# Optimization experiments

Hardware: AMD Instinct MI355X
Metric: run time of the kernel (lower is better)

Reference implementation:

```python
import jax, jax.numpy as jnp
import numpy as np

N = 50000
NEG_SLOPE = 0.2


def add_self_loops(edge_index, n):
    loop = jnp.arange(n, dtype=edge_index.dtype)
    return jnp.concatenate([edge_index, jnp.stack([loop, loop])], axis=1)


def gatv2_conv(x, edge_index, Wl, bl, Wr, br, att, bias):
    """PyG GATv2Conv (share_weights=False, concat=True, add_self_loops applied by caller).
    x: [N, Fin]; edge_index: [2, E] with row0=src(j), row1=dst(i); att: [H, D].
    Returns (out [N, H*D], alpha [E, H])."""
    src, dst = edge_index[0], edge_index[1]
    H, D = att.shape
    n = x.shape[0]
    xl = (x @ Wl + bl).reshape(n, H, D)   # source-side transform
    xr = (x @ Wr + br).reshape(n, H, D)   # target-side transform
    e = jax.nn.leaky_relu(xl[src] + xr[dst], NEG_SLOPE)        # [E, H, D]
    logit = jnp.einsum('ehd,hd->eh', e, att)                    # [E, H]
    # segment softmax over edges grouped by target node
    lmax = jax.ops.segment_max(logit, dst, num_segments=n)      # [N, H]
    ex = jnp.exp(logit - lmax[dst])
    denom = jax.ops.segment_sum(ex, dst, num_segments=n)
    alpha = ex / denom[dst]                                     # [E, H]
    out = jax.ops.segment_sum(alpha[:, :, None] * xl[src], dst, num_segments=n)  # [N, H, D]
    return out.reshape(n, H * D) + bias, alpha


def setup_inputs() -> dict:
    key = jax.random.key(0)
    ks = jax.random.split(key, 16)
    E = 400000
    x = jax.random.normal(ks[0], (N, 23), dtype=jnp.float32)
    edge_index = jax.random.randint(ks[1], (2, E), 0, N, dtype=jnp.int64)
    H1, D1 = 8, 64
    F1 = H1 * D1  # 512
    s = 0.1
    return {
        'x': x,
        'edge_index': edge_index,
        'Wl1': jax.random.normal(ks[2], (23, F1), dtype=jnp.float32) * s,
        'bl1': jnp.zeros((F1,), jnp.float32),
        'Wr1': jax.random.normal(ks[3], (23, F1), dtype=jnp.float32) * s,
        'br1': jnp.zeros((F1,), jnp.float32),
        'att1': jax.random.normal(ks[4], (H1, D1), dtype=jnp.float32) * s,
        'bias1': jnp.zeros((F1,), jnp.float32),
        'Wl2': jax.random.normal(ks[5], (F1, 1), dtype=jnp.float32) * s,
        'bl2': jnp.zeros((1,), jnp.float32),
        'Wr2': jax.random.normal(ks[6], (F1, 1), dtype=jnp.float32) * s,
        'br2': jnp.zeros((1,), jnp.float32),
        'att2': jax.random.normal(ks[7], (1, 1), dtype=jnp.float32) * s,
        'bias2': jnp.zeros((1,), jnp.float32),
    }


def reference(x, edge_index, Wl1, bl1, Wr1, br1, att1, bias1,
              Wl2, bl2, Wr2, br2, att2, bias2):
    ei = add_self_loops(edge_index, N)
    h, _ = gatv2_conv(x, ei, Wl1, bl1, Wr1, br1, att1, bias1)
    h = jax.nn.relu(h)
    h, alpha = gatv2_conv(h, ei, Wl2, bl2, Wr2, br2, att2, bias2)
    return h, alpha
```

## Files before the change

kernel.cpp:

```cpp
#include <hip/hip_runtime.h>
#include <math.h>

#define NN 50000
#define E0 400000
#define EE 450000
#define FF 512
#define G1 2048
#define NPB 25
#define EPB 220
#define WAVES_TOTAL (G1 * 4)
#define MAXD 64
#define LOG2E 1.44269504f

typedef _Float16 h2 __attribute__((ext_vector_type(2)));

__device__ __forceinline__ h2 uas_h2(unsigned u) { union { unsigned u; h2 h; } c; c.u = u; return c.h; }
__device__ __forceinline__ unsigned h2as_u(h2 h) { union { unsigned u; h2 h; } c; c.h = h; return c.u; }
__device__ __forceinline__ unsigned packh(float a, float b) {
    h2 hh = { (_Float16)a, (_Float16)b };
    return h2as_u(hh);
}
__device__ __forceinline__ float leaky(float v) { return fmaxf(v, 0.2f * v); }

__global__ __launch_bounds__(256) void k_predeg(
    const float* __restrict__ x,
    const float* __restrict__ Wl1, const float* __restrict__ bl1,
    const float* __restrict__ Wr1, const float* __restrict__ br1,
    const int* __restrict__ ei,
    unsigned* __restrict__ xlh, unsigned* __restrict__ xrh,
    int* __restrict__ cnt, int* __restrict__ src_sl)
{
    __shared__ unsigned sxh[NPB * 12];
    int b = blockIdx.x, t = threadIdx.x;

    {
        int e0 = b * EPB;
        int e1 = e0 + EPB; if (e1 > EE) e1 = EE;
        for (int e = e0 + t; e < e1; e += 256) {
            int src, dst;
            if (e < E0) { src = ei[e]; dst = ei[E0 + e]; }
            else        { src = e - E0; dst = src; }
            int p = atomicAdd(&cnt[dst], 1);
            if (p < MAXD) src_sl[(size_t)dst * MAXD + p] = src;
        }
    }

    int i0 = b * NPB;
    int i1 = i0 + NPB; if (i1 > NN) i1 = NN;
    int nnod = i1 - i0;
    for (int k = t; k < nnod * 12; k += 256) {
        int n = k / 12, j = k - n * 12;
        const float* row = x + (size_t)(i0 + n) * 23;
        float f0 = row[2 * j];
        float f1 = (2 * j + 1 < 23) ? row[2 * j + 1] : 0.f;
        sxh[n * 12 + j] = packh(f0, f1);
    }

    int c0 = 2 * t, c1 = 2 * t + 1;
    h2 wl0[12], wl1[12], wr0[12], wr1[12];
#pragma unroll
    for (int j = 0; j < 12; j++) {
        int r0 = 2 * j, r1 = 2 * j + 1;
        float a, b2;
        a = Wl1[r0 * FF + c0]; b2 = (r1 < 23) ? Wl1[r1 * FF + c0] : 0.f;
        wl0[j] = (h2){ (_Float16)a, (_Float16)b2 };
        a = Wl1[r0 * FF + c1]; b2 = (r1 < 23) ? Wl1[r1 * FF + c1] : 0.f;
        wl1[j] = (h2){ (_Float16)a, (_Float16)b2 };
        a = Wr1[r0 * FF + c0]; b2 = (r1 < 23) ? Wr1[r1 * FF + c0] : 0.f;
        wr0[j] = (h2){ (_Float16)a, (_Float16)b2 };
        a = Wr1[r0 * FF + c1]; b2 = (r1 < 23) ? Wr1[r1 * FF + c1] : 0.f;
        wr1[j] = (h2){ (_Float16)a, (_Float16)b2 };
    }
    float bl0 = bl1[c0], bl1s = bl1[c1];
    float br0 = br1[c0], br1s = br1[c1];
    __syncthreads();

    const uint4* S = (const uint4*)sxh;
    for (int n = 0; n < nnod; n++) {
        uint4 xa = S[n * 3 + 0];
        uint4 xb = S[n * 3 + 1];
        uint4 xc = S[n * 3 + 2];
        h2 xv[12] = { uas_h2(xa.x), uas_h2(xa.y), uas_h2(xa.z), uas_h2(xa.w),
                      uas_h2(xb.x), uas_h2(xb.y), uas_h2(xb.z), uas_h2(xb.w),
                      uas_h2(xc.x), uas_h2(xc.y), uas_h2(xc.z), uas_h2(xc.w) };
        float al0 = bl0, al1 = bl1s, ar0 = br0, ar1 = br1s;
#pragma unroll
        for (int j = 0; j < 12; j++) {
            al0 = __builtin_amdgcn_fdot2(wl0[j], xv[j], al0, false);
            al1 = __builtin_amdgcn_fdot2(wl1[j], xv[j], al1, false);
            ar0 = __builtin_amdgcn_fdot2(wr0[j], xv[j], ar0, false);
            ar1 = __builtin_amdgcn_fdot2(wr1[j], xv[j], ar1, false);
        }
        xlh[(size_t)(i0 + n) * 256 + t] = packh(al0, al1);
        xrh[(size_t)(i0 + n) * 256 + t] = packh(ar0, ar1);
    }
}

__global__ __launch_bounds__(256) void k_layer1(
    const uint4* __restrict__ xlh, const uint4* __restrict__ xrh,
    const float* __restrict__ att, const float* __restrict__ bias1,
    const float* __restrict__ Wl2, const float* __restrict__ bl2,
    const float* __restrict__ Wr2, const float* __restrict__ br2,
    const int* __restrict__ cnt, const int* __restrict__ src_sl,
    float* __restrict__ xl2, float* __restrict__ xr2)
{
    int t = threadIdx.x;
    int l = t & 63;
    int wid = blockIdx.x * 4 + (t >> 6);

    float4 atA = ((const float4*)att)[2 * l];
    float4 atB = ((const float4*)att)[2 * l + 1];
    h2 a6_0 = { (_Float16)(0.6f * LOG2E * atA.x), (_Float16)(0.6f * LOG2E * atA.y) };
    h2 a6_1 = { (_Float16)(0.6f * LOG2E * atA.z), (_Float16)(0.6f * LOG2E * atA.w) };
    h2 a6_2 = { (_Float16)(0.6f * LOG2E * atB.x), (_Float16)(0.6f * LOG2E * atB.y) };
    h2 a6_3 = { (_Float16)(0.6f * LOG2E * atB.z), (_Float16)(0.6f * LOG2E * atB.w) };
    h2 a4_0 = { (_Float16)(0.4f * LOG2E * atA.x), (_Float16)(0.4f * LOG2E * atA.y) };
    h2 a4_1 = { (_Float16)(0.4f * LOG2E * atA.z), (_Float16)(0.4f * LOG2E * atA.w) };
    h2 a4_2 = { (_Float16)(0.4f * LOG2E * atB.x), (_Float16)(0.4f * LOG2E * atB.y) };
    h2 a4_3 = { (_Float16)(0.4f * LOG2E * atB.z), (_Float16)(0.4f * LOG2E * atB.w) };
    float bl2v = bl2[0], br2v = br2[0];

    for (int i = wid; i < NN; i += WAVES_TOTAL) {
        uint4 xq = xrh[(size_t)i * 64 + l];
        h2 q0 = uas_h2(xq.x), q1 = uas_h2(xq.y), q2 = uas_h2(xq.z), q3 = uas_h2(xq.w);

        float s = 0.f;
        h2 A0 = { 0, 0 }, A1 = { 0, 0 }, A2 = { 0, 0 }, A3 = { 0, 0 };

        int dg = cnt[i]; if (dg > MAXD) dg = MAXD;
        int myj = (l < dg) ? src_sl[(size_t)i * MAXD + l] : 0;

        int j0 = __builtin_amdgcn_readlane(myj, 0);
        uint4 r0 = xlh[(size_t)j0 * 64 + l];
        uint4 r1 = r0;
        if (dg > 1) r1 = xlh[(size_t)__builtin_amdgcn_readlane(myj, 1) * 64 + l];

        for (int p = 0; p < dg; p++) {
            uint4 rn = r0;
            if (p + 2 < dg)
                rn = xlh[(size_t)__builtin_amdgcn_readlane(myj, p + 2) * 64 + l];

            h2 p0 = uas_h2(r0.x), p1 = uas_h2(r0.y), p2 = uas_h2(r0.z), p3 = uas_h2(r0.w);
            h2 t0 = p0 + q0, t1 = p1 + q1, t2 = p2 + q2, t3 = p3 + q3;
            h2 b0 = uas_h2(h2as_u(t0) & 0x7fff7fffu);
            h2 b1 = uas_h2(h2as_u(t1) & 0x7fff7fffu);
            h2 b2 = uas_h2(h2as_u(t2) & 0x7fff7fffu);
            h2 b3 = uas_h2(h2as_u(t3) & 0x7fff7fffu);
            float part = 0.f;
            part = __builtin_amdgcn_fdot2(a6_0, t0, part, false);
            part = __builtin_amdgcn_fdot2(a4_0, b0, part, false);
            part = __builtin_amdgcn_fdot2(a6_1, t1, part, false);
            part = __builtin_amdgcn_fdot2(a4_1, b1, part, false);
            part = __builtin_amdgcn_fdot2(a6_2, t2, part, false);
            part = __builtin_amdgcn_fdot2(a4_2, b2, part, false);
            part = __builtin_amdgcn_fdot2(a6_3, t3, part, false);
            part = __builtin_amdgcn_fdot2(a4_3, b3, part, false);
            part += __shfl_xor(part, 1, 64);
            part += __shfl_xor(part, 2, 64);
            part += __shfl_xor(part, 4, 64);
            float wv = exp2f(part);
            s += wv;
            _Float16 wh = (_Float16)wv;
            h2 w2 = { wh, wh };
            A0 += w2 * p0;
            A1 += w2 * p1;
            A2 += w2 * p2;
            A3 += w2 * p3;
            r0 = r1; r1 = rn;
        }

        float inv = 1.f / s;
        float4 bA = ((const float4*)bias1)[2 * l];
        float4 bB = ((const float4*)bias1)[2 * l + 1];
        float h0 = fmaxf(fmaf((float)A0[0], inv, bA.x), 0.f);
        float h1 = fmaxf(fmaf((float)A0[1], inv, bA.y), 0.f);
        float h2v = fmaxf(fmaf((float)A1[0], inv, bA.z), 0.f);
        float h3 = fmaxf(fmaf((float)A1[1], inv, bA.w), 0.f);
        float h4 = fmaxf(fmaf((float)A2[0], inv, bB.x), 0.f);
        float h5 = fmaxf(fmaf((float)A2[1], inv, bB.y), 0.f);
        float h6 = fmaxf(fmaf((float)A3[0], inv, bB.z), 0.f);
        float h7 = fmaxf(fmaf((float)A3[1], inv, bB.w), 0.f);

        float4 wlA = ((const float4*)Wl2)[2 * l];
        float4 wlB = ((const float4*)Wl2)[2 * l + 1];
        float4 wrA = ((const float4*)Wr2)[2 * l];
        float4 wrB = ((const float4*)Wr2)[2 * l + 1];
        float pl = h0 * wlA.x + h1 * wlA.y + h2v * wlA.z + h3 * wlA.w
                 + h4 * wlB.x + h5 * wlB.y + h6 * wlB.z + h7 * wlB.w;
        float pr = h0 * wrA.x + h1 * wrA.y + h2v * wrA.z + h3 * wrA.w
                 + h4 * wrB.x + h5 * wrB.y + h6 * wrB.z + h7 * wrB.w;
#pragma unroll
        for (int o = 32; o > 0; o >>= 1) {
            pl += __shfl_xor(pl, o, 64);
            pr += __shfl_xor(pr, o, 64);
        }
        if (l == 0) {
            xl2[i] = pl + bl2v;
            xr2[i] = pr + br2v;
        }
    }
}

__global__ void k_layer2a(const float* __restrict__ xl2, const float* __restrict__ xr2,
                          const float* __restrict__ att2, const float* __restrict__ bias2,
                          const int* __restrict__ cnt, const int* __restrict__ src_sl,
                          float* __restrict__ out, float* __restrict__ invs)
{
    int i = blockIdx.x * blockDim.x + threadIdx.x;
    if (i >= NN) return;
    int dg = cnt[i]; if (dg > MAXD) dg = MAXD;
    const int* sp = src_sl + (size_t)i * MAXD;
    float xri = xr2[i];
    float a2l = att2[0] * LOG2E;
    float s = 0.f, num = 0.f;
    for (int p = 0; p < dg; p++) {
        float v = xl2[sp[p]];
        float w = exp2f(leaky(v + xri) * a2l);
        s += w;
        num = fmaf(w, v, num);
    }
    out[i] = num / s + bias2[0];
    invs[i] = 1.f / s;
}

__global__ void k_layer2b(const float* __restrict__ xl2, const float* __restrict__ xr2,
                          const float* __restrict__ att2, const int* __restrict__ ei,
                          const float* __restrict__ invs, float* __restrict__ out)
{
    int e = blockIdx.x * blockDim.x + threadIdx.x;
    if (e >= EE) return;
    int src, dst;
    if (e < E0) { src = ei[e]; dst = ei[E0 + e]; }
    else        { src = e - E0; dst = src; }
    float a2l = att2[0] * LOG2E;
    float lg = leaky(xl2[src] + xr2[dst]) * a2l;
    out[NN + e] = exp2f(lg) * invs[dst];
}

extern "C" void kernel_launch(void* const* d_in, const int* in_sizes, int n_in,
                              void* d_out, int out_size, void* d_ws, size_t ws_size,
                              hipStream_t stream)
{
    const float* x     = (const float*)d_in[0];
    const int*   ei    = (const int*)d_in[1];
    const float* Wl1   = (const float*)d_in[2];
    const float* bl1   = (const float*)d_in[3];
    const float* Wr1   = (const float*)d_in[4];
    const float* br1   = (const float*)d_in[5];
    const float* att1  = (const float*)d_in[6];
    const float* bias1 = (const float*)d_in[7];
    const float* Wl2   = (const float*)d_in[8];
    const float* bl2   = (const float*)d_in[9];
    const float* Wr2   = (const float*)d_in[10];
    const float* br2   = (const float*)d_in[11];
    const float* att2  = (const float*)d_in[12];
    const float* bias2 = (const float*)d_in[13];
    float* out = (float*)d_out;

    char* ws = (char*)d_ws;
    unsigned* xlh  = (unsigned*)ws; ws += (size_t)NN * 256 * 4;
    unsigned* xrh  = (unsigned*)ws; ws += (size_t)NN * 256 * 4;
    float* xl2     = (float*)ws;    ws += (size_t)NN * 4;
    float* xr2     = (float*)ws;    ws += (size_t)NN * 4;
    float* invs    = (float*)ws;    ws += (size_t)NN * 4;
    int* cnt       = (int*)ws;      ws += (size_t)NN * 4;
    int* src_sl    = (int*)ws;      ws += (size_t)NN * MAXD * 4;

    hipMemsetAsync(cnt, 0, (size_t)NN * 4, stream);

    k_predeg<<<G1, 256, 0, stream>>>(x, Wl1, bl1, Wr1, br1, ei, xlh, xrh,
                                     cnt, src_sl);
    k_layer1<<<G1, 256, 0, stream>>>((const uint4*)xlh, (const uint4*)xrh,
                                     att1, bias1, Wl2, bl2, Wr2, br2,
                                     cnt, src_sl, xl2, xr2);
    k_layer2a<<<(NN + 255) / 256, 256, 0, stream>>>(xl2, xr2, att2, bias2,
                                                    cnt, src_sl, out, invs);
    k_layer2b<<<(EE + 255) / 256, 256, 0, stream>>>(xl2, xr2, att2, ei, invs, out);
}
```

Baseline: 228.0 us.

## Quantize source-side features to int8 with per-node scale for gather

The source-side transform xl is now stored as int8 with one per-node float scale instead of fp16. This halves the bytes gathered per edge in the layer-1 aggregation. Values are dequantized in registers with a magic-number fp16 trick and then multiplied by the scale. This adds a shared-memory pass and per-node max reduction in the producer kernel, and trades accuracy for bandwidth.

```diff
diff --git a/kernel.cpp b/kernel.cpp
--- a/kernel.cpp
+++ b/kernel.cpp
@@ -27,11 +27,15 @@
     const float* __restrict__ Wl1, const float* __restrict__ bl1,
     const float* __restrict__ Wr1, const float* __restrict__ br1,
     const int* __restrict__ ei,
-    unsigned* __restrict__ xlh, unsigned* __restrict__ xrh,
+    unsigned short* __restrict__ xlq, float* __restrict__ xlsc,
+    unsigned* __restrict__ xrh,
     int* __restrict__ cnt, int* __restrict__ src_sl)
 {
     __shared__ unsigned sxh[NPB * 12];
+    __shared__ unsigned sal[NPB * 256];
+    __shared__ float swmax[NPB * 4];
     int b = blockIdx.x, t = threadIdx.x;
+    int l = t & 63, w = t >> 6;
 
     {
         int e0 = b * EPB;
@@ -91,13 +95,32 @@
             ar0 = __builtin_amdgcn_fdot2(wr0[j], xv[j], ar0, false);
             ar1 = __builtin_amdgcn_fdot2(wr1[j], xv[j], ar1, false);
         }
-        xlh[(size_t)(i0 + n) * 256 + t] = packh(al0, al1);
         xrh[(size_t)(i0 + n) * 256 + t] = packh(ar0, ar1);
+        sal[n * 256 + t] = packh(al0, al1);
+        float m = fmaxf(fabsf(al0), fabsf(al1));
+#pragma unroll
+        for (int o = 32; o > 0; o >>= 1) m = fmaxf(m, __shfl_xor(m, o, 64));
+        if (l == 0) swmax[n * 4 + w] = m;
+    }
+    __syncthreads();
+
+    for (int n = 0; n < nnod; n++) {
+        float rm = fmaxf(fmaxf(swmax[n * 4 + 0], swmax[n * 4 + 1]),
+                         fmaxf(swmax[n * 4 + 2], swmax[n * 4 + 3]));
+        rm = fmaxf(rm, 1e-8f);
+        float qi = 127.f / rm;
+        h2 alp = uas_h2(sal[n * 256 + t]);
+        int q0 = (int)rintf(fminf(fmaxf((float)alp[0] * qi, -127.f), 127.f));
+        int q1 = (int)rintf(fminf(fmaxf((float)alp[1] * qi, -127.f), 127.f));
+        xlq[(size_t)(i0 + n) * 256 + t] =
+            (unsigned short)((q0 & 0xFF) | ((q1 & 0xFF) << 8));
+        if (t == 0) xlsc[i0 + n] = rm * (1.f / 127.f);
     }
 }
 
 __global__ __launch_bounds__(256) void k_layer1(
-    const uint4* __restrict__ xlh, const uint4* __restrict__ xrh,
+    const unsigned char* __restrict__ xlq, const float* __restrict__ xlsc,
+    const uint4* __restrict__ xrh,
     const float* __restrict__ att, const float* __restrict__ bias1,
     const float* __restrict__ Wl2, const float* __restrict__ bl2,
     const float* __restrict__ Wr2, const float* __restrict__ br2,
@@ -118,11 +141,12 @@
     h2 a4_1 = { (_Float16)(0.4f * LOG2E * atA.z), (_Float16)(0.4f * LOG2E * atA.w) };
     h2 a4_2 = { (_Float16)(0.4f * LOG2E * atB.x), (_Float16)(0.4f * LOG2E * atB.y) };
     h2 a4_3 = { (_Float16)(0.4f * LOG2E * atB.z), (_Float16)(0.4f * LOG2E * atB.w) };
+    const h2 cm1152 = { (_Float16)(-1152.f), (_Float16)(-1152.f) };
     float bl2v = bl2[0], br2v = br2[0];
 
     for (int i = wid; i < NN; i += WAVES_TOTAL) {
         uint4 xq = xrh[(size_t)i * 64 + l];
-        h2 q0 = uas_h2(xq.x), q1 = uas_h2(xq.y), q2 = uas_h2(xq.z), q3 = uas_h2(xq.w);
+        h2 q0h = uas_h2(xq.x), q1h = uas_h2(xq.y), q2h = uas_h2(xq.z), q3h = uas_h2(xq.w);
 
         float s = 0.f;
         h2 A0 = { 0, 0 }, A1 = { 0, 0 }, A2 = { 0, 0 }, A3 = { 0, 0 };
@@ -131,17 +155,34 @@
         int myj = (l < dg) ? src_sl[(size_t)i * MAXD + l] : 0;
 
         int j0 = __builtin_amdgcn_readlane(myj, 0);
-        uint4 r0 = xlh[(size_t)j0 * 64 + l];
-        uint4 r1 = r0;
-        if (dg > 1) r1 = xlh[(size_t)__builtin_amdgcn_readlane(myj, 1) * 64 + l];
+        uint2 r0 = *(const uint2*)(xlq + (size_t)j0 * 512 + 8 * l);
+        float S0 = xlsc[j0];
+        uint2 r1 = r0; float S1 = S0;
+        if (dg > 1) {
+            int j1 = __builtin_amdgcn_readlane(myj, 1);
+            r1 = *(const uint2*)(xlq + (size_t)j1 * 512 + 8 * l);
+            S1 = xlsc[j1];
+        }
 
         for (int p = 0; p < dg; p++) {
-            uint4 rn = r0;
-            if (p + 2 < dg)
-                rn = xlh[(size_t)__builtin_amdgcn_readlane(myj, p + 2) * 64 + l];
-
-            h2 p0 = uas_h2(r0.x), p1 = uas_h2(r0.y), p2 = uas_h2(r0.z), p3 = uas_h2(r0.w);
-            h2 t0 = p0 + q0, t1 = p1 + q1, t2 = p2 + q2, t3 = p3 + q3;
+            uint2 rn = r0; float Sn = S0;
+            if (p + 2 < dg) {
+                int jn = __builtin_amdgcn_readlane(myj, p + 2);
+                rn = *(const uint2*)(xlq + (size_t)jn * 512 + 8 * l);
+                Sn = xlsc[jn];
+            }
+
+            unsigned ex = r0.x ^ 0x80808080u, ey = r0.y ^ 0x80808080u;
+            unsigned w0u = ((ex & 0xFFu) | ((ex << 8) & 0xFF0000u)) | 0x64006400u;
+            unsigned w1u = (((ex >> 16) & 0xFFu) | ((ex >> 8) & 0xFF0000u)) | 0x64006400u;
+            unsigned w2u = ((ey & 0xFFu) | ((ey << 8) & 0xFF0000u)) | 0x64006400u;
+            unsigned w3u = (((ey >> 16) & 0xFFu) | ((ey >> 8) & 0xFF0000u)) | 0x64006400u;
+            h2 qq0 = uas_h2(w0u) + cm1152, qq1 = uas_h2(w1u) + cm1152;
+            h2 qq2 = uas_h2(w2u) + cm1152, qq3 = uas_h2(w3u) + cm1152;
+            _Float16 Sh = (_Float16)S0;
+            h2 S2 = { Sh, Sh };
+            h2 v0 = qq0 * S2, v1 = qq1 * S2, v2 = qq2 * S2, v3 = qq3 * S2;
+            h2 t0 = v0 + q0h, t1 = v1 + q1h, t2 = v2 + q2h, t3 = v3 + q3h;
             h2 b0 = uas_h2(h2as_u(t0) & 0x7fff7fffu);
             h2 b1 = uas_h2(h2as_u(t1) & 0x7fff7fffu);
             h2 b2 = uas_h2(h2as_u(t2) & 0x7fff7fffu);
@@ -162,11 +203,11 @@
             s += wv;
             _Float16 wh = (_Float16)wv;
             h2 w2 = { wh, wh };
-            A0 += w2 * p0;
-            A1 += w2 * p1;
-            A2 += w2 * p2;
-            A3 += w2 * p3;
-            r0 = r1; r1 = rn;
+            A0 += w2 * v0;
+            A1 += w2 * v1;
+            A2 += w2 * v2;
+            A3 += w2 * v3;
+            r0 = r1; S0 = S1; r1 = rn; S1 = Sn;
         }
 
         float inv = 1.f / s;
@@ -258,7 +299,8 @@
     float* out = (float*)d_out;
 
     char* ws = (char*)d_ws;
-    unsigned* xlh  = (unsigned*)ws; ws += (size_t)NN * 256 * 4;
+    unsigned short* xlq = (unsigned short*)ws; ws += (size_t)NN * 512;
+    float* xlsc    = (float*)ws;    ws += (size_t)NN * 4;
     unsigned* xrh  = (unsigned*)ws; ws += (size_t)NN * 256 * 4;
     float* xl2     = (float*)ws;    ws += (size_t)NN * 4;
     float* xr2     = (float*)ws;    ws += (size_t)NN * 4;
@@ -268,9 +310,10 @@
 
     hipMemsetAsync(cnt, 0, (size_t)NN * 4, stream);
 
-    k_predeg<<<G1, 256, 0, stream>>>(x, Wl1, bl1, Wr1, br1, ei, xlh, xrh,
+    k_predeg<<<G1, 256, 0, stream>>>(x, Wl1, bl1, Wr1, br1, ei, xlq, xlsc, xrh,
                                      cnt, src_sl);
-    k_layer1<<<G1, 256, 0, stream>>>((const uint4*)xlh, (const uint4*)xrh,
+    k_layer1<<<G1, 256, 0, stream>>>((const unsigned char*)xlq, xlsc,
+                                     (const uint4*)xrh,
                                      att1, bias1, Wl2, bl2, Wr2, br2,
                                      cnt, src_sl, xl2, xr2);
     k_layer2a<<<(NN + 255) / 256, 256, 0, stream>>>(xl2, xr2, att2, bias2,
```

Result: slower. 244.2 us (+7.1%).

## Quantize layer-1 node features to int8 with per-node scales and unroll edge loop

Applied to the files above, without the earlier changes.

The fp16 source and target feature tables are replaced by int8 values with a per-node absmax scale, halving the bytes gathered per edge in the layer-1 aggregation. The edge loop is unrolled by two with dual accumulators and a deeper prefetch window. Dequantization uses a magic-number fp16 trick. This adds an extra block-wide reduction and __syncthreads per node in the precompute kernel, and it loses accuracy to int8 rounding.

```diff
diff --git a/kernel.cpp b/kernel.cpp
--- a/kernel.cpp
+++ b/kernel.cpp
@@ -27,11 +27,14 @@
     const float* __restrict__ Wl1, const float* __restrict__ bl1,
     const float* __restrict__ Wr1, const float* __restrict__ br1,
     const int* __restrict__ ei,
-    unsigned* __restrict__ xlh, unsigned* __restrict__ xrh,
+    unsigned short* __restrict__ xlq, float* __restrict__ xlsc,
+    unsigned short* __restrict__ xrq, float* __restrict__ xrsc,
     int* __restrict__ cnt, int* __restrict__ src_sl)
 {
     __shared__ unsigned sxh[NPB * 12];
+    __shared__ float swm[2][8];
     int b = blockIdx.x, t = threadIdx.x;
+    int l = t & 63, w = t >> 6;
 
     {
         int e0 = b * EPB;
@@ -91,13 +94,77 @@
             ar0 = __builtin_amdgcn_fdot2(wr0[j], xv[j], ar0, false);
             ar1 = __builtin_amdgcn_fdot2(wr1[j], xv[j], ar1, false);
         }
-        xlh[(size_t)(i0 + n) * 256 + t] = packh(al0, al1);
-        xrh[(size_t)(i0 + n) * 256 + t] = packh(ar0, ar1);
-    }
-}
+        float ml = fmaxf(fabsf(al0), fabsf(al1));
+        float mr = fmaxf(fabsf(ar0), fabsf(ar1));
+#pragma unroll
+        for (int o = 32; o > 0; o >>= 1) {
+            ml = fmaxf(ml, __shfl_xor(ml, o, 64));
+            mr = fmaxf(mr, __shfl_xor(mr, o, 64));
+        }
+        if (l == 0) { swm[n & 1][w] = ml; swm[n & 1][4 + w] = mr; }
+        __syncthreads();
+        float rml = fmaxf(fmaxf(swm[n & 1][0], swm[n & 1][1]),
+                          fmaxf(swm[n & 1][2], swm[n & 1][3]));
+        float rmr = fmaxf(fmaxf(swm[n & 1][4], swm[n & 1][5]),
+                          fmaxf(swm[n & 1][6], swm[n & 1][7]));
+        rml = fmaxf(rml, 1e-8f);
+        rmr = fmaxf(rmr, 1e-8f);
+        float qil = 127.f / rml, qir = 127.f / rmr;
+        int q0 = (int)rintf(fminf(fmaxf(al0 * qil, -127.f), 127.f));
+        int q1 = (int)rintf(fminf(fmaxf(al1 * qil, -127.f), 127.f));
+        int p0 = (int)rintf(fminf(fmaxf(ar0 * qir, -127.f), 127.f));
+        int p1 = (int)rintf(fminf(fmaxf(ar1 * qir, -127.f), 127.f));
+        xlq[(size_t)(i0 + n) * 256 + t] = (unsigned short)((q0 & 0xFF) | ((q1 & 0xFF) << 8));
+        xrq[(size_t)(i0 + n) * 256 + t] = (unsigned short)((p0 & 0xFF) | ((p1 & 0xFF) << 8));
+        if (t == 0) {
+            xlsc[i0 + n] = rml * (1.f / 127.f);
+            xrsc[i0 + n] = rmr * (1.f / 127.f);
+        }
+    }
+}
+
+#define EDGE_STEP(R, SJ, SACC, AA0, AA1, AA2, AA3)                               \
+    do {                                                                         \
+        unsigned ex = (R).x ^ 0x80808080u, ey = (R).y ^ 0x80808080u;             \
+        unsigned w0u = ((ex & 0xFFu) | ((ex << 8) & 0xFF0000u)) | 0x64006400u;   \
+        unsigned w1u = (((ex >> 16) & 0xFFu) | ((ex >> 8) & 0xFF0000u)) | 0x64006400u; \
+        unsigned w2u = ((ey & 0xFFu) | ((ey << 8) & 0xFF0000u)) | 0x64006400u;   \
+        unsigned w3u = (((ey >> 16) & 0xFFu) | ((ey >> 8) & 0xFF0000u)) | 0x64006400u; \
+        h2 qq0 = uas_h2(w0u) + cm1152, qq1 = uas_h2(w1u) + cm1152;               \
+        h2 qq2 = uas_h2(w2u) + cm1152, qq3 = uas_h2(w3u) + cm1152;               \
+        _Float16 Sh = (_Float16)(SJ);                                            \
+        h2 Ss = { Sh, Sh };                                                      \
+        h2 v0 = qq0 * Ss, v1 = qq1 * Ss, v2 = qq2 * Ss, v3 = qq3 * Ss;           \
+        h2 t0 = v0 + xp0, t1 = v1 + xp1, t2 = v2 + xp2, t3 = v3 + xp3;           \
+        h2 b0 = uas_h2(h2as_u(t0) & 0x7fff7fffu);                                \
+        h2 b1 = uas_h2(h2as_u(t1) & 0x7fff7fffu);                                \
+        h2 b2 = uas_h2(h2as_u(t2) & 0x7fff7fffu);                                \
+        h2 b3 = uas_h2(h2as_u(t3) & 0x7fff7fffu);                                \
+        float part = 0.f;                                                        \
+        part = __builtin_amdgcn_fdot2(a6_0, t0, part, false);                    \
+        part = __builtin_amdgcn_fdot2(a4_0, b0, part, false);                    \
+        part = __builtin_amdgcn_fdot2(a6_1, t1, part, false);                    \
+        part = __builtin_amdgcn_fdot2(a4_1, b1, part, false);                    \
+        part = __builtin_amdgcn_fdot2(a6_2, t2, part, false);                    \
+        part = __builtin_amdgcn_fdot2(a4_2, b2, part, false);                    \
+        part = __builtin_amdgcn_fdot2(a6_3, t3, part, false);                    \
+        part = __builtin_amdgcn_fdot2(a4_3, b3, part, false);                    \
+        part += __shfl_xor(part, 1, 64);                                         \
+        part += __shfl_xor(part, 2, 64);                                         \
+        part += __shfl_xor(part, 4, 64);                                         \
+        float wv = exp2f(part);                                                  \
+        (SACC) += wv;                                                            \
+        _Float16 wh = (_Float16)wv;                                              \
+        h2 w2h = { wh, wh };                                                     \
+        (AA0) += w2h * v0;                                                       \
+        (AA1) += w2h * v1;                                                       \
+        (AA2) += w2h * v2;                                                       \
+        (AA3) += w2h * v3;                                                       \
+    } while (0)
 
 __global__ __launch_bounds__(256) void k_layer1(
-    const uint4* __restrict__ xlh, const uint4* __restrict__ xrh,
+    const unsigned char* __restrict__ xlq, const float* __restrict__ xlsc,
+    const unsigned char* __restrict__ xrq, const float* __restrict__ xrsc,
     const float* __restrict__ att, const float* __restrict__ bias1,
     const float* __restrict__ Wl2, const float* __restrict__ bl2,
     const float* __restrict__ Wr2, const float* __restrict__ br2,
@@ -118,56 +185,62 @@
     h2 a4_1 = { (_Float16)(0.4f * LOG2E * atA.z), (_Float16)(0.4f * LOG2E * atA.w) };
     h2 a4_2 = { (_Float16)(0.4f * LOG2E * atB.x), (_Float16)(0.4f * LOG2E * atB.y) };
     h2 a4_3 = { (_Float16)(0.4f * LOG2E * atB.z), (_Float16)(0.4f * LOG2E * atB.w) };
+    const h2 cm1152 = { (_Float16)(-1152.f), (_Float16)(-1152.f) };
     float bl2v = bl2[0], br2v = br2[0];
 
     for (int i = wid; i < NN; i += WAVES_TOTAL) {
-        uint4 xq = xrh[(size_t)i * 64 + l];
-        h2 q0 = uas_h2(xq.x), q1 = uas_h2(xq.y), q2 = uas_h2(xq.z), q3 = uas_h2(xq.w);
-
-        float s = 0.f;
-        h2 A0 = { 0, 0 }, A1 = { 0, 0 }, A2 = { 0, 0 }, A3 = { 0, 0 };
+        uint2 xq = *(const uint2*)(xrq + (size_t)i * 512 + 8 * l);
+        float Sr = xrsc[i];
+        unsigned bx = xq.x ^ 0x80808080u, by = xq.y ^ 0x80808080u;
+        float f0 = __uint_as_float(0x4B000000u | (bx & 0xFFu)) - 8388736.f;
+        float f1 = __uint_as_float(0x4B000000u | ((bx >> 8) & 0xFFu)) - 8388736.f;
+        float f2 = __uint_as_float(0x4B000000u | ((bx >> 16) & 0xFFu)) - 8388736.f;
+        float f3 = __uint_as_float(0x4B000000u | ((bx >> 24) & 0xFFu)) - 8388736.f;
+        float f4 = __uint_as_float(0x4B000000u | (by & 0xFFu)) - 8388736.f;
+        float f5 = __uint_as_float(0x4B000000u | ((by >> 8) & 0xFFu)) - 8388736.f;
+        float f6 = __uint_as_float(0x4B000000u | ((by >> 16) & 0xFFu)) - 8388736.f;
+        float f7 = __uint_as_float(0x4B000000u | ((by >> 24) & 0xFFu)) - 8388736.f;
+        h2 xp0 = { (_Float16)(f0 * Sr), (_Float16)(f1 * Sr) };
+        h2 xp1 = { (_Float16)(f2 * Sr), (_Float16)(f3 * Sr) };
+        h2 xp2 = { (_Float16)(f4 * Sr), (_Float16)(f5 * Sr) };
+        h2 xp3 = { (_Float16)(f6 * Sr), (_Float16)(f7 * Sr) };
+
+        float sA = 0.f, sB = 0.f;
+        h2 A0a = { 0, 0 }, A1a = { 0, 0 }, A2a = { 0, 0 }, A3a = { 0, 0 };
+        h2 A0b = { 0, 0 }, A1b = { 0, 0 }, A2b = { 0, 0 }, A3b = { 0, 0 };
 
         int dg = cnt[i]; if (dg > MAXD) dg = MAXD;
         int myj = (l < dg) ? src_sl[(size_t)i * MAXD + l] : 0;
 
         int j0 = __builtin_amdgcn_readlane(myj, 0);
-        uint4 r0 = xlh[(size_t)j0 * 64 + l];
-        uint4 r1 = r0;
-        if (dg > 1) r1 = xlh[(size_t)__builtin_amdgcn_readlane(myj, 1) * 64 + l];
-
-        for (int p = 0; p < dg; p++) {
-            uint4 rn = r0;
-            if (p + 2 < dg)
-                rn = xlh[(size_t)__builtin_amdgcn_readlane(myj, p + 2) * 64 + l];
-
-            h2 p0 = uas_h2(r0.x), p1 = uas_h2(r0.y), p2 = uas_h2(r0.z), p3 = uas_h2(r0.w);
-            h2 t0 = p0 + q0, t1 = p1 + q1, t2 = p2 + q2, t3 = p3 + q3;
-            h2 b0 = uas_h2(h2as_u(t0) & 0x7fff7fffu);
-            h2 b1 = uas_h2(h2as_u(t1) & 0x7fff7fffu);
-            h2 b2 = uas_h2(h2as_u(t2) & 0x7fff7fffu);
-            h2 b3 = uas_h2(h2as_u(t3) & 0x7fff7fffu);
-            float part = 0.f;
-            part = __builtin_amdgcn_fdot2(a6_0, t0, part, false);
-            part = __builtin_amdgcn_fdot2(a4_0, b0, part, false);
-            part = __builtin_amdgcn_fdot2(a6_1, t1, part, false);
-            part = __builtin_amdgcn_fdot2(a4_1, b1, part, false);
-            part = __builtin_amdgcn_fdot2(a6_2, t2, part, false);
-            part = __builtin_amdgcn_fdot2(a4_2, b2, part, false);
-            part = __builtin_amdgcn_fdot2(a6_3, t3, part, false);
-            part = __builtin_amdgcn_fdot2(a4_3, b3, part, false);
-            part += __shfl_xor(part, 1, 64);
-            part += __shfl_xor(part, 2, 64);
-            part += __shfl_xor(part, 4, 64);
-            float wv = exp2f(part);
-            s += wv;
-            _Float16 wh = (_Float16)wv;
-            h2 w2 = { wh, wh };
-            A0 += w2 * p0;
-            A1 += w2 * p1;
-            A2 += w2 * p2;
-            A3 += w2 * p3;
-            r0 = r1; r1 = rn;
-        }
+        uint2 r0 = *(const uint2*)(xlq + (size_t)j0 * 512 + 8 * l);
+        float g0 = xlsc[j0];
+        uint2 r1 = r0, r2 = r0, r3 = r0;
+        float g1 = g0, g2 = g0, g3 = g0;
+        if (dg > 1) { int j = __builtin_amdgcn_readlane(myj, 1);
+                      r1 = *(const uint2*)(xlq + (size_t)j * 512 + 8 * l); g1 = xlsc[j]; }
+        if (dg > 2) { int j = __builtin_amdgcn_readlane(myj, 2);
+                      r2 = *(const uint2*)(xlq + (size_t)j * 512 + 8 * l); g2 = xlsc[j]; }
+        if (dg > 3) { int j = __builtin_amdgcn_readlane(myj, 3);
+                      r3 = *(const uint2*)(xlq + (size_t)j * 512 + 8 * l); g3 = xlsc[j]; }
+
+        int p = 0;
+        for (; p + 2 <= dg; p += 2) {
+            uint2 n0 = r0, n1 = r0;
+            float h0s = g0, h1s = g0;
+            if (p + 4 < dg) { int j = __builtin_amdgcn_readlane(myj, p + 4);
+                              n0 = *(const uint2*)(xlq + (size_t)j * 512 + 8 * l); h0s = xlsc[j]; }
+            if (p + 5 < dg) { int j = __builtin_amdgcn_readlane(myj, p + 5);
+                              n1 = *(const uint2*)(xlq + (size_t)j * 512 + 8 * l); h1s = xlsc[j]; }
+            EDGE_STEP(r0, g0, sA, A0a, A1a, A2a, A3a);
+            EDGE_STEP(r1, g1, sB, A0b, A1b, A2b, A3b);
+            r0 = r2; g0 = g2; r1 = r3; g1 = g3;
+            r2 = n0; g2 = h0s; r3 = n1; g3 = h1s;
+        }
+        if (p < dg) EDGE_STEP(r0, g0, sA, A0a, A1a, A2a, A3a);
+
+        float s = sA + sB;
+        h2 A0 = A0a + A0b, A1 = A1a + A1b, A2 = A2a + A2b, A3 = A3a + A3b;
 
         float inv = 1.f / s;
         float4 bA = ((const float4*)bias1)[2 * l];
@@ -258,8 +331,10 @@
     float* out = (float*)d_out;
 
     char* ws = (char*)d_ws;
-    unsigned* xlh  = (unsigned*)ws; ws += (size_t)NN * 256 * 4;
-    unsigned* xrh  = (unsigned*)ws; ws += (size_t)NN * 256 * 4;
+    unsigned short* xlq = (unsigned short*)ws; ws += (size_t)NN * 512;
+    unsigned short* xrq = (unsigned short*)ws; ws += (size_t)NN * 512;
+    float* xlsc    = (float*)ws;    ws += (size_t)NN * 4;
+    float* xrsc    = (float*)ws;    ws += (size_t)NN * 4;
     float* xl2     = (float*)ws;    ws += (size_t)NN * 4;
     float* xr2     = (float*)ws;    ws += (size_t)NN * 4;
     float* invs    = (float*)ws;    ws += (size_t)NN * 4;
@@ -268,9 +343,10 @@
 
     hipMemsetAsync(cnt, 0, (size_t)NN * 4, stream);
 
-    k_predeg<<<G1, 256, 0, stream>>>(x, Wl1, bl1, Wr1, br1, ei, xlh, xrh,
-                                     cnt, src_sl);
-    k_layer1<<<G1, 256, 0, stream>>>((const uint4*)xlh, (const uint4*)xrh,
+    k_predeg<<<G1, 256, 0, stream>>>(x, Wl1, bl1, Wr1, br1, ei,
+                                     xlq, xlsc, xrq, xrsc, cnt, src_sl);
+    k_layer1<<<G1, 256, 0, stream>>>((const unsigned char*)xlq, xlsc,
+                                     (const unsigned char*)xrq, xrsc,
                                      att1, bias1, Wl2, bl2, Wr2, br2,
                                      cnt, src_sl, xl2, xr2);
     k_layer2a<<<(NN + 255) / 256, 256, 0, stream>>>(xl2, xr2, att2, bias2,
```

After: 263.1 us. 15.4% more time.
